# Kernel tuning notes

Hardware: AMD Instinct MI355X
Metric: run time of the kernel (lower is better)

Reference implementation:

```python
import jax, jax.numpy as jnp
import numpy as np

DIM, BIN = 128, 16
LN_EPS = 1e-5


def setup_inputs() -> dict:
    key = jax.random.key(0)
    ks = jax.random.split(key, 16)
    B, Ld, Lc, O = 4096, 50, 50, 64
    D_VOCAB, C_VOCAB = 100000, 1000
    inp = {
        "discrete_index": jax.random.randint(ks[0], (B, Ld), 0, D_VOCAB, dtype=jnp.int32),
        "discrete_mask": jax.random.randint(ks[1], (B, Ld), 0, 2, dtype=jnp.int32),
        "continue_value": jax.random.normal(ks[2], (B, Lc), dtype=jnp.float32),
        "continue_index": jax.random.randint(ks[3], (B, Lc), 0, C_VOCAB, dtype=jnp.int32),
        "continue_mask": jax.random.randint(ks[4], (B, Lc), 0, 2, dtype=jnp.int32),
        # learned parameters (last row = padding idx, zeroed like torch padding_idx init semantics)
        "disc_emb": jax.random.normal(ks[5], (D_VOCAB + 1, DIM), dtype=jnp.float32).at[D_VOCAB].set(0.0),
        "v_emb": jax.random.normal(ks[6], (C_VOCAB + 1, BIN), dtype=jnp.float32).at[C_VOCAB].set(0.0),
        "b1_emb": jax.random.normal(ks[7], (C_VOCAB + 1, BIN), dtype=jnp.float32).at[C_VOCAB].set(0.0),
        "w_emb": jax.random.normal(ks[8], (C_VOCAB + 1, DIM * BIN), dtype=jnp.float32).at[C_VOCAB].set(0.0),
        "b2_emb": jax.random.normal(ks[9], (C_VOCAB + 1, DIM), dtype=jnp.float32).at[C_VOCAB].set(0.0),
        "ln_gamma": jnp.ones((BIN,), dtype=jnp.float32),
        "ln_beta": jnp.zeros((BIN,), dtype=jnp.float32),
        "transform_matrix": jax.random.normal(ks[10], (O, Ld + Lc), dtype=jnp.float32),
    }
    return inp


def reference(discrete_index, discrete_mask, continue_value, continue_index, continue_mask,
              disc_emb, v_emb, b1_emb, w_emb, b2_emb, ln_gamma, ln_beta, transform_matrix):
    B, Lc = continue_index.shape
    # embedding gathers
    discrete_part = disc_emb[discrete_index]            # [B, Ld, D]
    v = v_emb[continue_index]                           # [B, Lc, BIN]
    b1 = b1_emb[continue_index]                         # [B, Lc, BIN]
    w = w_emb[continue_index].reshape(B, Lc, BIN, DIM)  # [B, Lc, BIN, D]
    b2 = b2_emb[continue_index]                         # [B, Lc, D]
    # per-token mini-MLP: LayerNorm(bin) + ReLU + bmm with per-token weight
    h = continue_value[..., None] * v + b1              # [B, Lc, BIN]
    mu = jnp.mean(h, axis=-1, keepdims=True)
    var = jnp.mean((h - mu) ** 2, axis=-1, keepdims=True)
    hn = (h - mu) * jax.lax.rsqrt(var + LN_EPS) * ln_gamma + ln_beta
    a = jax.nn.relu(hn)
    continuous_part = jnp.einsum('blk,blkd->bld', a, w) + b2  # [B, Lc, D]
    parts = jnp.concatenate([discrete_part, continuous_part], axis=1)  # [B, L, D]
    out = jnp.einsum('ol,bld->bod', transform_matrix, parts)           # [B, O, D]
    # mask (no-grad path in original)
    mvec = jnp.concatenate([1 - discrete_mask, 1 - continue_mask], axis=1).astype(jnp.float32)  # [B, L]
    full_mask = (1.0 - jnp.sign(jnp.einsum('ol,bl->bo', transform_matrix, mvec))).astype(jnp.int32)  # [B, O]
    return out, full_mask
```

## Files before the change

kernel.cpp:

```cpp
#include <hip/hip_runtime.h>
#include <hip/hip_bf16.h>

#define NB 4096
#define LD_ 50
#define LC_ 50
#define LTOT 100
#define DIM 128
#define BIN 16
#define NO 64
#define KPAD 128
#define LP 136
#define LN_EPS 1e-5f

typedef __attribute__((ext_vector_type(8))) short bf16x8;
typedef __attribute__((ext_vector_type(4))) float f32x4;

__device__ __forceinline__ unsigned short f2bf(float f) {
    return __builtin_bit_cast(unsigned short, __float2bfloat16(f));
}
__device__ __forceinline__ float bf2f(unsigned u16) {
    return __builtin_bit_cast(float, u16 << 16);
}

__global__ __launch_bounds__(256) void convW_kernel(const float* __restrict__ w,
                                                    unsigned short* __restrict__ wbf) {
    int t = blockIdx.x * 256 + threadIdx.x;
    float4 v = *reinterpret_cast<const float4*>(w + (size_t)t * 4);
    unsigned lo = (unsigned)f2bf(v.x) | ((unsigned)f2bf(v.y) << 16);
    unsigned hi = (unsigned)f2bf(v.z) | ((unsigned)f2bf(v.w) << 16);
    *reinterpret_cast<uint2*>(wbf + (size_t)t * 4) = make_uint2(lo, hi);
}

__global__ __launch_bounds__(256) void convT_kernel(const float* __restrict__ T,
                                                    unsigned short* __restrict__ Tbf) {
    int t = blockIdx.x * 256 + threadIdx.x;
    if (t < NO * KPAD) {
        int o = t >> 7, k = t & 127;
        float v = (k < LTOT) ? T[o * LTOT + k] : 0.f;
        Tbf[t] = f2bf(v);
    }
}

__global__ __launch_bounds__(256) void fused_embed_kernel(
    const int* __restrict__ dindex,
    const int* __restrict__ dmask,
    const float* __restrict__ cval,
    const int* __restrict__ cindex,
    const int* __restrict__ cmask,
    const float* __restrict__ disc_emb,
    const float* __restrict__ v_emb,
    const float* __restrict__ b1_emb,
    const unsigned short* __restrict__ w_bf,
    const float* __restrict__ b2_emb,
    const float* __restrict__ ln_gamma,
    const float* __restrict__ ln_beta,
    const float* __restrict__ T,
    const unsigned short* __restrict__ Tbf,
    float* __restrict__ out,
    float* __restrict__ outmask)
{
    __shared__ unsigned short PbfT[DIM * LP];
    __shared__ float buf32[4][2][DIM];
    __shared__ float mvec[LTOT];

    const int b    = blockIdx.x;
    const int tid  = threadIdx.x;
    const int wave = tid >> 6;
    const int lane = tid & 63;

    if (tid < LTOT) {
        int m = (tid < LD_) ? dmask[b * LD_ + tid] : cmask[b * LC_ + (tid - LD_)];
        mvec[tid] = 1.0f - (float)m;
    }

    {
        const int d  = tid & 127;
        const int hh = tid >> 7;
        unsigned short* row = &PbfT[d * LP];
        if (hh == 0) {
            #pragma unroll
            for (int q = 0; q < 4; ++q)
                *reinterpret_cast<uint2*>(&row[100 + q * 4]) = make_uint2(0u, 0u);
        } else {
            #pragma unroll
            for (int q = 0; q < 3; ++q)
                *reinterpret_cast<uint2*>(&row[116 + q * 4]) = make_uint2(0u, 0u);
        }
    }

    {
        const int d  = tid & 127;
        const int hh = tid >> 7;
        for (int q = hh; q < 12; q += 2) {
            const int l0 = q * 4;
            float f[4];
            #pragma unroll
            for (int j = 0; j < 4; ++j) {
                int idx = dindex[b * LD_ + l0 + j];
                f[j] = disc_emb[(size_t)idx * DIM + d];
            }
            unsigned lo = (unsigned)f2bf(f[0]) | ((unsigned)f2bf(f[1]) << 16);
            unsigned hi = (unsigned)f2bf(f[2]) | ((unsigned)f2bf(f[3]) << 16);
            *reinterpret_cast<uint2*>(&PbfT[d * LP + l0]) = make_uint2(lo, hi);
        }
        if (hh == 0) {
            float f0 = disc_emb[(size_t)dindex[b * LD_ + 48] * DIM + d];
            float f1 = disc_emb[(size_t)dindex[b * LD_ + 49] * DIM + d];
            *reinterpret_cast<unsigned int*>(&PbfT[d * LP + 48]) =
                (unsigned)f2bf(f0) | ((unsigned)f2bf(f1) << 16);
        }
    }

    {
        const int th = lane >> 5;
        const int q  = lane & 31;
        const int bcast = lane & 32;

        for (int p = wave; p < 25; p += 4) {
            const int t  = p * 2 + th;
            const int ci = cindex[b * LC_ + t];
            const float cv = cval[b * LC_ + t];

            float a_val = 0.f;
            if (q < 16) {
                float h = cv * v_emb[ci * BIN + q] + b1_emb[ci * BIN + q];
                float s = h;
                s += __shfl_xor(s, 1, 16);
                s += __shfl_xor(s, 2, 16);
                s += __shfl_xor(s, 4, 16);
                s += __shfl_xor(s, 8, 16);
                float mu = s * (1.f / BIN);
                float e  = h - mu;
                float v2 = e * e;
                v2 += __shfl_xor(v2, 1, 16);
                v2 += __shfl_xor(v2, 2, 16);
                v2 += __shfl_xor(v2, 4, 16);
                v2 += __shfl_xor(v2, 8, 16);
                float rstd = rsqrtf(v2 * (1.f / BIN) + LN_EPS);
                a_val = fmaxf(e * rstd * ln_gamma[q] + ln_beta[q], 0.f);
            }

            float4 acc = *reinterpret_cast<const float4*>(b2_emb + (size_t)ci * DIM + q * 4);
            const uint2* wp = reinterpret_cast<const uint2*>(w_bf + (size_t)ci * (BIN * DIM) + q * 4);
            #pragma unroll
            for (int k = 0; k < BIN; ++k) {
                float ak = __shfl(a_val, bcast + k);
                uint2 wv = wp[k * 32];
                acc.x += ak * bf2f(wv.x & 0xffffu);
                acc.y += ak * bf2f(wv.x >> 16);
                acc.z += ak * bf2f(wv.y & 0xffffu);
                acc.w += ak * bf2f(wv.y >> 16);
            }

            *reinterpret_cast<float4*>(&buf32[wave][th][q * 4]) = acc;
            __builtin_amdgcn_wave_barrier();
            float x0 = buf32[wave][0][lane];
            float x1 = buf32[wave][1][lane];
            float x2 = buf32[wave][0][lane + 64];
            float x3 = buf32[wave][1][lane + 64];
            __builtin_amdgcn_wave_barrier();
            const int l0 = 50 + p * 2;
            *reinterpret_cast<unsigned int*>(&PbfT[lane * LP + l0]) =
                (unsigned)f2bf(x0) | ((unsigned)f2bf(x1) << 16);
            *reinterpret_cast<unsigned int*>(&PbfT[(lane + 64) * LP + l0]) =
                (unsigned)f2bf(x2) | ((unsigned)f2bf(x3) << 16);
        }
    }

    __syncthreads();

    if (tid < NO) {
        float s = 0.f;
        for (int l = 0; l < LTOT; ++l) s += T[tid * LTOT + l] * mvec[l];
        float sg = (s > 0.f) ? 1.f : ((s < 0.f) ? -1.f : 0.f);
        outmask[(size_t)b * NO + tid] = 1.f - sg;
    }

    {
        const int r16 = lane & 15;
        const int g4  = lane >> 4;

        f32x4 acc[8];
        #pragma unroll
        for (int nt = 0; nt < 8; ++nt) acc[nt] = (f32x4){0.f, 0.f, 0.f, 0.f};

        bf16x8 afr[4];
        const unsigned short* Ta = Tbf + (16 * wave + r16) * KPAD + g4 * 8;
        #pragma unroll
        for (int kc = 0; kc < 4; ++kc)
            afr[kc] = *reinterpret_cast<const bf16x8*>(Ta + kc * 32);

        #pragma unroll
        for (int nt = 0; nt < 8; ++nt) {
            const unsigned short* Bp = &PbfT[(nt * 16 + r16) * LP + g4 * 8];
            #pragma unroll
            for (int kc = 0; kc < 4; ++kc) {
                bf16x8 bfr = *reinterpret_cast<const bf16x8*>(Bp + kc * 32);
                acc[nt] = __builtin_amdgcn_mfma_f32_16x16x32_bf16(afr[kc], bfr, acc[nt], 0, 0, 0);
            }
        }

        float* ob = out + (size_t)b * NO * DIM + (size_t)(16 * wave) * DIM;
        #pragma unroll
        for (int nt = 0; nt < 8; ++nt) {
            #pragma unroll
            for (int r = 0; r < 4; ++r) {
                ob[(g4 * 4 + r) * DIM + nt * 16 + r16] = acc[nt][r];
            }
        }
    }
}

extern "C" void kernel_launch(void* const* d_in, const int* in_sizes, int n_in,
                              void* d_out, int out_size, void* d_ws, size_t ws_size,
                              hipStream_t stream) {
    const int*   dindex  = (const int*)  d_in[0];
    const int*   dmask   = (const int*)  d_in[1];
    const float* cval    = (const float*)d_in[2];
    const int*   cindex  = (const int*)  d_in[3];
    const int*   cmask   = (const int*)  d_in[4];
    const float* disc_emb= (const float*)d_in[5];
    const float* v_emb   = (const float*)d_in[6];
    const float* b1_emb  = (const float*)d_in[7];
    const float* w_emb   = (const float*)d_in[8];
    const float* b2_emb  = (const float*)d_in[9];
    const float* lng     = (const float*)d_in[10];
    const float* lnb     = (const float*)d_in[11];
    const float* T       = (const float*)d_in[12];

    float* out     = (float*)d_out;
    float* outmask = out + (size_t)NB * NO * DIM;

    unsigned short* w_bf = (unsigned short*)d_ws;
    unsigned short* Tbf  = (unsigned short*)((char*)d_ws + 4100096);

    hipLaunchKernelGGL(convW_kernel, dim3(2002), dim3(256), 0, stream, w_emb, w_bf);
    hipLaunchKernelGGL(convT_kernel, dim3(32), dim3(256), 0, stream, T, Tbf);
    hipLaunchKernelGGL(fused_embed_kernel, dim3(NB), dim3(256), 0, stream,
                       dindex, dmask, cval, cindex, cmask,
                       disc_emb, v_emb, b1_emb, w_bf, b2_emb,
                       lng, lnb, T, Tbf, out, outmask);
}
```

Baseline: 323.5 us.

## Pre-convert discrete embedding table to bf16 and use 512-thread blocks

```diff
diff --git a/kernel.cpp b/kernel.cpp
--- a/kernel.cpp
+++ b/kernel.cpp
@@ -12,42 +12,68 @@
 #define LP 136
 #define LN_EPS 1e-5f
 
+#define DISC_ELEMS 12800128
+#define DISC_VEC8  1600016
+#define DISC_BLKS  6251
+#define W_VEC8     256256
+#define W_BLKS     1001
+#define T_BLKS     32
+#define CONV_BLKS  (DISC_BLKS + W_BLKS + T_BLKS)
+
 typedef __attribute__((ext_vector_type(8))) short bf16x8;
 typedef __attribute__((ext_vector_type(4))) float f32x4;
 
-__device__ __forceinline__ unsigned short f2bf(float f) {
-    return __builtin_bit_cast(unsigned short, __float2bfloat16(f));
+__device__ __forceinline__ unsigned f2bf(float f) {
+    return (unsigned)__builtin_bit_cast(unsigned short, __float2bfloat16(f));
 }
 __device__ __forceinline__ float bf2f(unsigned u16) {
     return __builtin_bit_cast(float, u16 << 16);
 }
 
-__global__ __launch_bounds__(256) void convW_kernel(const float* __restrict__ w,
-                                                    unsigned short* __restrict__ wbf) {
-    int t = blockIdx.x * 256 + threadIdx.x;
-    float4 v = *reinterpret_cast<const float4*>(w + (size_t)t * 4);
-    unsigned lo = (unsigned)f2bf(v.x) | ((unsigned)f2bf(v.y) << 16);
-    unsigned hi = (unsigned)f2bf(v.z) | ((unsigned)f2bf(v.w) << 16);
-    *reinterpret_cast<uint2*>(wbf + (size_t)t * 4) = make_uint2(lo, hi);
-}
-
-__global__ __launch_bounds__(256) void convT_kernel(const float* __restrict__ T,
-                                                    unsigned short* __restrict__ Tbf) {
-    int t = blockIdx.x * 256 + threadIdx.x;
-    if (t < NO * KPAD) {
+__global__ __launch_bounds__(256) void conv_all(const float* __restrict__ disc,
+                                                const float* __restrict__ w,
+                                                const float* __restrict__ T,
+                                                unsigned short* __restrict__ disc_bf,
+                                                unsigned short* __restrict__ w_bf,
+                                                unsigned short* __restrict__ Tbf) {
+    const int bb = blockIdx.x;
+    if (bb < DISC_BLKS) {
+        size_t v = (size_t)bb * 256 + threadIdx.x;
+        if (v < DISC_VEC8) {
+            const float4* src = reinterpret_cast<const float4*>(disc + v * 8);
+            float4 a = src[0], c = src[1];
+            uint4 o;
+            o.x = f2bf(a.x) | (f2bf(a.y) << 16);
+            o.y = f2bf(a.z) | (f2bf(a.w) << 16);
+            o.z = f2bf(c.x) | (f2bf(c.y) << 16);
+            o.w = f2bf(c.z) | (f2bf(c.w) << 16);
+            *reinterpret_cast<uint4*>(disc_bf + v * 8) = o;
+        }
+    } else if (bb < DISC_BLKS + W_BLKS) {
+        size_t v = (size_t)(bb - DISC_BLKS) * 256 + threadIdx.x;
+        const float4* src = reinterpret_cast<const float4*>(w + v * 8);
+        float4 a = src[0], c = src[1];
+        uint4 o;
+        o.x = f2bf(a.x) | (f2bf(a.y) << 16);
+        o.y = f2bf(a.z) | (f2bf(a.w) << 16);
+        o.z = f2bf(c.x) | (f2bf(c.y) << 16);
+        o.w = f2bf(c.z) | (f2bf(c.w) << 16);
+        *reinterpret_cast<uint4*>(w_bf + v * 8) = o;
+    } else {
+        int t = (bb - DISC_BLKS - W_BLKS) * 256 + threadIdx.x;
         int o = t >> 7, k = t & 127;
         float v = (k < LTOT) ? T[o * LTOT + k] : 0.f;
-        Tbf[t] = f2bf(v);
-    }
-}
-
-__global__ __launch_bounds__(256) void fused_embed_kernel(
+        Tbf[t] = (unsigned short)f2bf(v);
+    }
+}
+
+__global__ __launch_bounds__(512, 6) void fused_embed_kernel(
     const int* __restrict__ dindex,
     const int* __restrict__ dmask,
     const float* __restrict__ cval,
     const int* __restrict__ cindex,
     const int* __restrict__ cmask,
-    const float* __restrict__ disc_emb,
+    const unsigned short* __restrict__ disc_bf,
     const float* __restrict__ v_emb,
     const float* __restrict__ b1_emb,
     const unsigned short* __restrict__ w_bf,
@@ -60,13 +86,15 @@
     float* __restrict__ outmask)
 {
     __shared__ unsigned short PbfT[DIM * LP];
-    __shared__ float buf32[4][2][DIM];
+    __shared__ float buf32[8][2][DIM];
     __shared__ float mvec[LTOT];
 
     const int b    = blockIdx.x;
     const int tid  = threadIdx.x;
     const int wave = tid >> 6;
     const int lane = tid & 63;
+    const int d    = tid & 127;
+    const int hh   = tid >> 7;
 
     if (tid < LTOT) {
         int m = (tid < LD_) ? dmask[b * LD_ + tid] : cmask[b * LC_ + (tid - LD_)];
@@ -74,56 +102,77 @@
     }
 
     {
-        const int d  = tid & 127;
-        const int hh = tid >> 7;
         unsigned short* row = &PbfT[d * LP];
+        if (hh < 3) {
+            *reinterpret_cast<uint2*>(&row[100 + hh * 8])     = make_uint2(0u, 0u);
+            *reinterpret_cast<uint2*>(&row[100 + hh * 8 + 4]) = make_uint2(0u, 0u);
+        } else {
+            *reinterpret_cast<uint2*>(&row[124]) = make_uint2(0u, 0u);
+        }
+    }
+
+    {
+        int idxs[12];
+        #pragma unroll
+        for (int i = 0; i < 3; ++i) {
+            const int l0 = (hh + 4 * i) * 4;
+            #pragma unroll
+            for (int j = 0; j < 4; ++j)
+                idxs[i * 4 + j] = dindex[b * LD_ + l0 + j];
+        }
+        int it0 = 0, it1 = 0;
+        if (hh == 0) { it0 = dindex[b * LD_ + 48]; it1 = dindex[b * LD_ + 49]; }
+
+        unsigned short u[12];
+        #pragma unroll
+        for (int i = 0; i < 12; ++i)
+            u[i] = disc_bf[(size_t)idxs[i] * DIM + d];
+        unsigned short ut0 = 0, ut1 = 0;
         if (hh == 0) {
-            #pragma unroll
-            for (int q = 0; q < 4; ++q)
-                *reinterpret_cast<uint2*>(&row[100 + q * 4]) = make_uint2(0u, 0u);
-        } else {
-            #pragma unroll
-            for (int q = 0; q < 3; ++q)
-                *reinterpret_cast<uint2*>(&row[116 + q * 4]) = make_uint2(0u, 0u);
-        }
-    }
-
-    {
-        const int d  = tid & 127;
-        const int hh = tid >> 7;
-        for (int q = hh; q < 12; q += 2) {
-            const int l0 = q * 4;
-            float f[4];
-            #pragma unroll
-            for (int j = 0; j < 4; ++j) {
-                int idx = dindex[b * LD_ + l0 + j];
-                f[j] = disc_emb[(size_t)idx * DIM + d];
-            }
-            unsigned lo = (unsigned)f2bf(f[0]) | ((unsigned)f2bf(f[1]) << 16);
-            unsigned hi = (unsigned)f2bf(f[2]) | ((unsigned)f2bf(f[3]) << 16);
+            ut0 = disc_bf[(size_t)it0 * DIM + d];
+            ut1 = disc_bf[(size_t)it1 * DIM + d];
+        }
+
+        #pragma unroll
+        for (int i = 0; i < 3; ++i) {
+            const int l0 = (hh + 4 * i) * 4;
+            unsigned lo = (unsigned)u[i*4+0] | ((unsigned)u[i*4+1] << 16);
+            unsigned hi = (unsigned)u[i*4+2] | ((unsigned)u[i*4+3] << 16);
             *reinterpret_cast<uint2*>(&PbfT[d * LP + l0]) = make_uint2(lo, hi);
         }
         if (hh == 0) {
-            float f0 = disc_emb[(size_t)dindex[b * LD_ + 48] * DIM + d];
-            float f1 = disc_emb[(size_t)dindex[b * LD_ + 49] * DIM + d];
             *reinterpret_cast<unsigned int*>(&PbfT[d * LP + 48]) =
-                (unsigned)f2bf(f0) | ((unsigned)f2bf(f1) << 16);
-        }
-    }
-
-    {
-        const int th = lane >> 5;
-        const int q  = lane & 31;
+                (unsigned)ut0 | ((unsigned)ut1 << 16);
+        }
+    }
+
+    {
+        const int th    = lane >> 5;
+        const int q     = lane & 31;
         const int bcast = lane & 32;
 
-        for (int p = wave; p < 25; p += 4) {
-            const int t  = p * 2 + th;
-            const int ci = cindex[b * LC_ + t];
-            const float cv = cval[b * LC_ + t];
+        int   ci[4];
+        float cv[4];
+        #pragma unroll
+        for (int j = 0; j < 4; ++j) {
+            const int p = wave + 8 * j;
+            if (p < 25) {
+                const int t = p * 2 + th;
+                ci[j] = cindex[b * LC_ + t];
+                cv[j] = cval[b * LC_ + t];
+            }
+        }
+
+        #pragma unroll
+        for (int j = 0; j < 4; ++j) {
+            const int p = wave + 8 * j;
+            if (p >= 25) break;
+            const int   c  = ci[j];
+            const float v0 = cv[j];
 
             float a_val = 0.f;
             if (q < 16) {
-                float h = cv * v_emb[ci * BIN + q] + b1_emb[ci * BIN + q];
+                float h = v0 * v_emb[c * BIN + q] + b1_emb[c * BIN + q];
                 float s = h;
                 s += __shfl_xor(s, 1, 16);
                 s += __shfl_xor(s, 2, 16);
@@ -140,8 +189,8 @@
                 a_val = fmaxf(e * rstd * ln_gamma[q] + ln_beta[q], 0.f);
             }
 
-            float4 acc = *reinterpret_cast<const float4*>(b2_emb + (size_t)ci * DIM + q * 4);
-            const uint2* wp = reinterpret_cast<const uint2*>(w_bf + (size_t)ci * (BIN * DIM) + q * 4);
+            float4 acc = *reinterpret_cast<const float4*>(b2_emb + (size_t)c * DIM + q * 4);
+            const uint2* wp = reinterpret_cast<const uint2*>(w_bf + (size_t)c * (BIN * DIM) + q * 4);
             #pragma unroll
             for (int k = 0; k < BIN; ++k) {
                 float ak = __shfl(a_val, bcast + k);
@@ -161,9 +210,9 @@
             __builtin_amdgcn_wave_barrier();
             const int l0 = 50 + p * 2;
             *reinterpret_cast<unsigned int*>(&PbfT[lane * LP + l0]) =
-                (unsigned)f2bf(x0) | ((unsigned)f2bf(x1) << 16);
+                f2bf(x0) | (f2bf(x1) << 16);
             *reinterpret_cast<unsigned int*>(&PbfT[(lane + 64) * LP + l0]) =
-                (unsigned)f2bf(x2) | ((unsigned)f2bf(x3) << 16);
+                f2bf(x2) | (f2bf(x3) << 16);
         }
     }
 
@@ -177,22 +226,24 @@
     }
 
     {
+        const int ot  = wave >> 1;
+        const int nh  = wave & 1;
         const int r16 = lane & 15;
         const int g4  = lane >> 4;
 
-        f32x4 acc[8];
-        #pragma unroll
-        for (int nt = 0; nt < 8; ++nt) acc[nt] = (f32x4){0.f, 0.f, 0.f, 0.f};
+        f32x4 acc[4];
+        #pragma unroll
+        for (int nt = 0; nt < 4; ++nt) acc[nt] = (f32x4){0.f, 0.f, 0.f, 0.f};
 
         bf16x8 afr[4];
-        const unsigned short* Ta = Tbf + (16 * wave + r16) * KPAD + g4 * 8;
+        const unsigned short* Ta = Tbf + (16 * ot + r16) * KPAD + g4 * 8;
         #pragma unroll
         for (int kc = 0; kc < 4; ++kc)
             afr[kc] = *reinterpret_cast<const bf16x8*>(Ta + kc * 32);
 
         #pragma unroll
-        for (int nt = 0; nt < 8; ++nt) {
-            const unsigned short* Bp = &PbfT[(nt * 16 + r16) * LP + g4 * 8];
+        for (int nt = 0; nt < 4; ++nt) {
+            const unsigned short* Bp = &PbfT[((nh * 4 + nt) * 16 + r16) * LP + g4 * 8];
             #pragma unroll
             for (int kc = 0; kc < 4; ++kc) {
                 bf16x8 bfr = *reinterpret_cast<const bf16x8*>(Bp + kc * 32);
@@ -200,9 +251,9 @@
             }
         }
 
-        float* ob = out + (size_t)b * NO * DIM + (size_t)(16 * wave) * DIM;
-        #pragma unroll
-        for (int nt = 0; nt < 8; ++nt) {
+        float* ob = out + (size_t)b * NO * DIM + (size_t)(16 * ot) * DIM + nh * 64;
+        #pragma unroll
+        for (int nt = 0; nt < 4; ++nt) {
             #pragma unroll
             for (int r = 0; r < 4; ++r) {
                 ob[(g4 * 4 + r) * DIM + nt * 16 + r16] = acc[nt][r];
@@ -231,13 +282,14 @@
     float* out     = (float*)d_out;
     float* outmask = out + (size_t)NB * NO * DIM;
 
-    unsigned short* w_bf = (unsigned short*)d_ws;
-    unsigned short* Tbf  = (unsigned short*)((char*)d_ws + 4100096);
-
-    hipLaunchKernelGGL(convW_kernel, dim3(2002), dim3(256), 0, stream, w_emb, w_bf);
-    hipLaunchKernelGGL(convT_kernel, dim3(32), dim3(256), 0, stream, T, Tbf);
-    hipLaunchKernelGGL(fused_embed_kernel, dim3(NB), dim3(256), 0, stream,
+    unsigned short* disc_bf = (unsigned short*)d_ws;
+    unsigned short* w_bf    = (unsigned short*)((char*)d_ws + 25600256);
+    unsigned short* Tbf     = (unsigned short*)((char*)d_ws + 25600256 + 4100096);
+
+    hipLaunchKernelGGL(conv_all, dim3(CONV_BLKS), dim3(256), 0, stream,
+                       disc_emb, w_emb, T, disc_bf, w_bf, Tbf);
+    hipLaunchKernelGGL(fused_embed_kernel, dim3(NB), dim3(512), 0, stream,
                        dindex, dmask, cval, cindex, cmask,
-                       disc_emb, v_emb, b1_emb, w_bf, b2_emb,
+                       disc_bf, v_emb, b1_emb, w_bf, b2_emb,
                        lng, lnb, T, Tbf, out, outmask);
 }
```

Measured after the change: 322.4 us. About the same (-0.3%).
